# Kernel optimization log

Measured on AMD Instinct MI355X. Metric: run time of the kernel, lower is better.

## Reference

```python
import jax, jax.numpy as jnp
import numpy as np

B, S, D, H = 2, 2048, 1024, 16
HD = D // H
SCALE = HD ** -0.5

def setup_inputs() -> dict:
    key = jax.random.key(0)
    ks = jax.random.split(key, 3)
    x = jax.random.normal(ks[0], (B, S, D), dtype=jnp.float32)
    Wqkv = jax.random.normal(ks[1], (D, 3 * D), dtype=jnp.float32) * (D ** -0.5)
    bqkv = jnp.zeros((3 * D,), dtype=jnp.float32)
    Wproj = jax.random.normal(ks[2], (D, D), dtype=jnp.float32) * (D ** -0.5)
    bproj = jnp.zeros((D,), dtype=jnp.float32)
    return {"x": x, "Wqkv": Wqkv, "bqkv": bqkv, "Wproj": Wproj, "bproj": bproj}

def reference(x, Wqkv, bqkv, Wproj, bproj):
    b, s, d = x.shape
    qkv = x @ Wqkv + bqkv                       # (b, s, 3d)
    qkv = qkv.reshape(b, s, 3, H, HD)
    q, k, v = (qkv[:, :, 0], qkv[:, :, 1], qkv[:, :, 2])  # (b, s, h, hd)
    # scores: (b, h, s, s)
    attn = jnp.einsum('bqhd,bkhd->bhqk', q, k) * SCALE
    attn = jax.nn.softmax(attn, axis=-1)
    out = jnp.einsum('bhqk,bkhd->bqhd', attn, v).reshape(b, s, d)
    out = out @ Wproj + bproj
    return out
```

## Files before the change

### kernel.cpp

```cpp
#include <hip/hip_runtime.h>

typedef __attribute__((ext_vector_type(8))) short bf16x8;
typedef __attribute__((ext_vector_type(4))) float f32x4;
typedef __attribute__((ext_vector_type(16))) float f32x16;
typedef unsigned short u16;
typedef unsigned int u32;

#define MFMA16(a,b,c) __builtin_amdgcn_mfma_f32_16x16x32_bf16((a),(b),(c),0,0,0)
#define MFMA32(a,b,c) __builtin_amdgcn_mfma_f32_32x32x16_bf16((a),(b),(c),0,0,0)

#if __has_builtin(__builtin_amdgcn_exp2f)
#define EXP2(x) __builtin_amdgcn_exp2f(x)
#else
#define EXP2(x) __expf((x) * 0.6931471805599453f)
#endif

__device__ __forceinline__ u16 f2bf(float f) {
  u32 u = __builtin_bit_cast(u32, f);
  u += 0x7FFFu + ((u >> 16) & 1u);
  return (u16)(u >> 16);
}

__device__ __forceinline__ u32 cvtpk(float lo, float hi) {
  u32 r;
  asm("v_cvt_pk_bf16_f32 %0, %1, %2" : "=v"(r) : "v"(lo), "v"(hi));
  return r;
}

__device__ __forceinline__ void swap32(u32& a, u32& b) {
#if __has_builtin(__builtin_amdgcn_permlane32_swap)
  auto r = __builtin_amdgcn_permlane32_swap((int)a, (int)b, false, false);
  a = (u32)r[0];
  b = (u32)r[1];
#else
  u32 pa = __shfl_xor(a, 32), pb = __shfl_xor(b, 32);
  bool lo = ((threadIdx.x & 32) == 0);
  u32 na = lo ? a : pb;
  u32 nb = lo ? pa : b;
  a = na; b = nb;
#endif
}

__device__ __forceinline__ void gload16(const u16* g, u16* l) {
  __builtin_amdgcn_global_load_lds(
      (const __attribute__((address_space(1))) u32*)(const void*)g,
      (__attribute__((address_space(3))) u32*)(void*)l, 16, 0, 0);
}

__device__ __forceinline__ bf16x8 ldsfrag(const u16* lds, int row, int chunk) {
  return *(const bf16x8*)(lds + row * 64 + ((chunk ^ (row & 7)) << 3));
}

__global__ __launch_bounds__(256) void convert_x(const float* __restrict__ in,
                                                 u16* __restrict__ out, int n4) {
  int i = blockIdx.x * blockDim.x + threadIdx.x;
  int stride = gridDim.x * blockDim.x;
  for (; i < n4; i += stride) {
    float4 v = ((const float4*)in)[i];
    u32 lo = (u32)f2bf(v.x) | ((u32)f2bf(v.y) << 16);
    u32 hi = (u32)f2bf(v.z) | ((u32)f2bf(v.w) << 16);
    uint2 pv; pv.x = lo; pv.y = hi;
    ((uint2*)out)[i] = pv;
  }
}

__global__ __launch_bounds__(256) void transpose_w(const float* __restrict__ in,
                                                   u16* __restrict__ out,
                                                   int R, int C) {
  __shared__ float t[32][33];
  int c0 = blockIdx.x * 32, r0 = blockIdx.y * 32;
  int tc = threadIdx.x & 31, tr = threadIdx.x >> 5;
#pragma unroll
  for (int j = 0; j < 4; ++j) {
    int r = tr + j * 8;
    t[r][tc] = in[(size_t)(r0 + r) * C + c0 + tc];
  }
  __syncthreads();
#pragma unroll
  for (int j = 0; j < 4; ++j) {
    int cc = tr + j * 8;
    out[(size_t)(c0 + cc) * R + r0 + tc] = f2bf(t[tc][cc]);
  }
}

template <int MODE>
__global__ __launch_bounds__(256, 3) void gemm_k(
    const u16* __restrict__ A, const u16* __restrict__ Bt,
    const float* __restrict__ bias,
    u16* __restrict__ Qo, u16* __restrict__ Ko, u16* __restrict__ Vt,
    float* __restrict__ Of) {
  __shared__ alignas(16) u16 As[3][4096];
  __shared__ alignas(16) u16 Bs[3][4096];
  const int tid = threadIdx.x;
  const int wid = tid >> 6, lane = tid & 63;
  const int g = lane >> 4, lr = lane & 15;
  const int m0 = blockIdx.y * 128, n0 = blockIdx.x * 128;
  const int wr = (wid >> 1) * 64, wc = (wid & 1) * 64;

  f32x4 acc[4][4];
#pragma unroll
  for (int i = 0; i < 4; ++i)
#pragma unroll
    for (int j = 0; j < 4; ++j) acc[i][j] = (f32x4){0.f, 0.f, 0.f, 0.f};

  const u16* Ab = A + (size_t)m0 * 1024;
  const u16* Bb = Bt + (size_t)n0 * 1024;

  const int srow = tid >> 2, sc = tid & 3;
  auto stage = [&](int buf, int kt) {
#pragma unroll
    for (int i = 0; i < 2; ++i) {
      int s = tid + i * 256;
      int row = srow + i * 64;
      int csrc = sc ^ ((row >> 1) & 3);
      gload16(Ab + (size_t)row * 1024 + kt + csrc * 8, As[buf] + s * 8);
      gload16(Bb + (size_t)row * 1024 + kt + csrc * 8, Bs[buf] + s * 8);
    }
  };

  stage(0, 0);
  stage(1, 32);
  int cur = 0;
  for (int ki = 0; ki < 32; ++ki) {
    if (ki + 2 < 32) {
      int nxt = cur + 2; if (nxt >= 3) nxt -= 3;
      stage(nxt, (ki + 2) * 32);
    }
    if (ki < 30)       asm volatile("s_waitcnt vmcnt(8)" ::: "memory");
    else if (ki == 30) asm volatile("s_waitcnt vmcnt(4)" ::: "memory");
    else               asm volatile("s_waitcnt vmcnt(0)" ::: "memory");
    __builtin_amdgcn_sched_barrier(0);
    __builtin_amdgcn_s_barrier();
    __builtin_amdgcn_sched_barrier(0);

    bf16x8 af[4], bfr[4];
#pragma unroll
    for (int i = 0; i < 4; ++i) {
      int row = wr + i * 16 + lr;
      int slot = g ^ ((row >> 1) & 3);
      af[i] = *(const bf16x8*)(As[cur] + row * 32 + slot * 8);
    }
#pragma unroll
    for (int j = 0; j < 4; ++j) {
      int row = wc + j * 16 + lr;
      int slot = g ^ ((row >> 1) & 3);
      bfr[j] = *(const bf16x8*)(Bs[cur] + row * 32 + slot * 8);
    }
    __builtin_amdgcn_s_setprio(1);
#pragma unroll
    for (int i = 0; i < 4; ++i)
#pragma unroll
      for (int j = 0; j < 4; ++j)
        acc[i][j] = MFMA16(af[i], bfr[j], acc[i][j]);
    __builtin_amdgcn_s_setprio(0);

    __builtin_amdgcn_s_barrier();
    __builtin_amdgcn_sched_barrier(0);
    cur += 1; if (cur >= 3) cur -= 3;
  }

  if constexpr (MODE == 1) {
#pragma unroll
    for (int i = 0; i < 4; ++i) {
      int row = m0 + wr + i * 16 + g * 4;
#pragma unroll
      for (int j = 0; j < 4; ++j) {
        int col = n0 + wc + j * 16 + lr;
        float bv = bias[col];
#pragma unroll
        for (int r = 0; r < 4; ++r)
          Of[(size_t)(row + r) * 1024 + col] = acc[i][j][r] + bv;
      }
    }
  } else {
    const int sel = n0 >> 10;
#pragma unroll
    for (int i = 0; i < 4; ++i) {
      int row = m0 + wr + i * 16 + g * 4;
      int b = row >> 11, s = row & 2047;
#pragma unroll
      for (int j = 0; j < 4; ++j) {
        int col = n0 + wc + j * 16 + lr;
        float bv = bias[col];
        int nn = col & 1023;
        int h = nn >> 6, hd = nn & 63;
        if (sel == 2) {
          u16 pk[4];
#pragma unroll
          for (int r = 0; r < 4; ++r) pk[r] = f2bf(acc[i][j][r] + bv);
          uint2 pv;
          pv.x = (u32)pk[0] | ((u32)pk[1] << 16);
          pv.y = (u32)pk[2] | ((u32)pk[3] << 16);
          *(uint2*)(Vt + (size_t)((b * 16 + h) * 64 + hd) * 2048 + s) = pv;
        } else {
          u16* dst = (sel == 0) ? Qo : Ko;
#pragma unroll
          for (int r = 0; r < 4; ++r)
            dst[(size_t)((b * 16 + h) * 2048 + s + r) * 64 + hd] =
                f2bf(acc[i][j][r] + bv);
        }
      }
    }
  }
}

__global__ __launch_bounds__(256, 2) void attn_k(const u16* __restrict__ Q,
                                                 const u16* __restrict__ K,
                                                 const u16* __restrict__ Vt,
                                                 u16* __restrict__ O) {
  __shared__ alignas(16) u16 Ks[3][4096];
  __shared__ alignas(16) u16 Vs[3][4096];
  const int tid = threadIdx.x;
  const int wid = tid >> 6, lane = tid & 63;
  const int l31 = lane & 31, b5 = lane >> 5;
  const int p = blockIdx.x;
  const int l = (p & 7) * 64 + (p >> 3);
  const int qt = l & 15, bh = l >> 4;
  const u16* Qh = Q + (size_t)bh * 2048 * 64;
  const u16* Kh = K + (size_t)bh * 2048 * 64;
  const u16* Vh = Vt + (size_t)bh * 64 * 2048;

  const int qbase = qt * 128 + wid * 32;
  const u16* qp = Qh + (size_t)(qbase + l31) * 64 + b5 * 8;
  bf16x8 qf[4];
#pragma unroll
  for (int c = 0; c < 4; ++c) qf[c] = *(const bf16x8*)(qp + 16 * c);
  __builtin_amdgcn_sched_barrier(0);

  auto stage = [&](int buf, int t) {
#pragma unroll
    for (int i = 0; i < 2; ++i) {
      int s = tid + i * 256;
      int row = s >> 3, c = (s & 7) ^ (row & 7);
      gload16(Kh + (t * 64 + row) * 64 + c * 8, Ks[buf] + s * 8);
      gload16(Vh + row * 2048 + t * 64 + c * 8, Vs[buf] + s * 8);
    }
  };
  stage(0, 0);
  stage(1, 1);

  f32x16 accO0, accO1;
#pragma unroll
  for (int r = 0; r < 16; ++r) { accO0[r] = 0.f; accO1[r] = 0.f; }
  float mraw = -1e30f;
  float mC = 0.f;
  float lsum = 0.f;

  const float C2 = 0.125f * 1.44269504088896f;

  int cur = 0;
  for (int t = 0; t < 32; ++t) {
    if (t + 2 < 32) {
      int nxt = cur + 2; if (nxt >= 3) nxt -= 3;
      stage(nxt, t + 2);
    }
    if (t < 30)       asm volatile("s_waitcnt vmcnt(8)" ::: "memory");
    else if (t == 30) asm volatile("s_waitcnt vmcnt(4)" ::: "memory");
    else              asm volatile("s_waitcnt vmcnt(0)" ::: "memory");
    __builtin_amdgcn_sched_barrier(0);
    __builtin_amdgcn_s_barrier();
    __builtin_amdgcn_sched_barrier(0);

    const u16* Kc = Ks[cur];
    const u16* Vc = Vs[cur];

    f32x16 s0, s1;
#pragma unroll
    for (int r = 0; r < 16; ++r) { s0[r] = 0.f; s1[r] = 0.f; }
    __builtin_amdgcn_s_setprio(1);
#pragma unroll
    for (int c = 0; c < 4; ++c) {
      bf16x8 k0 = ldsfrag(Kc, l31, 2 * c + b5);
      bf16x8 k1 = ldsfrag(Kc, 32 + l31, 2 * c + b5);
      s0 = MFMA32(k0, qf[c], s0);
      s1 = MFMA32(k1, qf[c], s1);
    }
    __builtin_amdgcn_s_setprio(0);

    float rmax;
    {
      float a0 = fmaxf(fmaxf(s0[0], s0[1]), fmaxf(s0[2], s0[3]));
      float a1 = fmaxf(fmaxf(s0[4], s0[5]), fmaxf(s0[6], s0[7]));
      float a2 = fmaxf(fmaxf(s0[8], s0[9]), fmaxf(s0[10], s0[11]));
      float a3 = fmaxf(fmaxf(s0[12], s0[13]), fmaxf(s0[14], s0[15]));
      float b0 = fmaxf(fmaxf(s1[0], s1[1]), fmaxf(s1[2], s1[3]));
      float b1 = fmaxf(fmaxf(s1[4], s1[5]), fmaxf(s1[6], s1[7]));
      float b2 = fmaxf(fmaxf(s1[8], s1[9]), fmaxf(s1[10], s1[11]));
      float b3 = fmaxf(fmaxf(s1[12], s1[13]), fmaxf(s1[14], s1[15]));
      rmax = fmaxf(fmaxf(fmaxf(a0, a1), fmaxf(a2, a3)),
                   fmaxf(fmaxf(b0, b1), fmaxf(b2, b3)));
    }
    rmax = fmaxf(rmax, __shfl_xor(rmax, 32));

    if (__any(rmax > mraw + 64.f)) {
      float mn = fmaxf(mraw, rmax);
      float al = EXP2((mraw - mn) * C2);
      mraw = mn;
      mC = mn * C2;
      lsum *= al;
#pragma unroll
      for (int r = 0; r < 16; ++r) {
        accO0[r] *= al;
        accO1[r] *= al;
      }
    }

    u32 w0[8], w1[8];
#pragma unroll
    for (int i = 0; i < 8; ++i) {
      float p0 = EXP2(__builtin_fmaf(s0[2 * i], C2, -mC));
      float p1 = EXP2(__builtin_fmaf(s0[2 * i + 1], C2, -mC));
      float p2 = EXP2(__builtin_fmaf(s1[2 * i], C2, -mC));
      float p3 = EXP2(__builtin_fmaf(s1[2 * i + 1], C2, -mC));
      lsum += (p0 + p1) + (p2 + p3);
      w0[i] = cvtpk(p0, p1);
      w1[i] = cvtpk(p2, p3);
    }

    __builtin_amdgcn_s_setprio(1);
#pragma unroll
    for (int c = 0; c < 4; ++c) {
      u32 a0, a1, b0, b1;
      if (c == 0)      { a0 = w0[0]; b0 = w0[2]; a1 = w0[1]; b1 = w0[3]; }
      else if (c == 1) { a0 = w0[4]; b0 = w0[6]; a1 = w0[5]; b1 = w0[7]; }
      else if (c == 2) { a0 = w1[0]; b0 = w1[2]; a1 = w1[1]; b1 = w1[3]; }
      else             { a0 = w1[4]; b0 = w1[6]; a1 = w1[5]; b1 = w1[7]; }
      swap32(a0, b0);
      swap32(a1, b1);
      uint4 u; u.x = a0; u.y = a1; u.z = b0; u.w = b1;
      bf16x8 pf = __builtin_bit_cast(bf16x8, u);
      bf16x8 v0 = ldsfrag(Vc, l31, 2 * c + b5);
      bf16x8 v1 = ldsfrag(Vc, 32 + l31, 2 * c + b5);
      accO0 = MFMA32(v0, pf, accO0);
      accO1 = MFMA32(v1, pf, accO1);
    }
    __builtin_amdgcn_s_setprio(0);

    __builtin_amdgcn_s_barrier();
    __builtin_amdgcn_sched_barrier(0);
    cur += 1; if (cur >= 3) cur -= 3;
  }

  float ls = lsum + __shfl_xor(lsum, 32);
  float inv = 1.f / ls;
  const int b = bh >> 4, h = bh & 15;
  u16* orow = O + (size_t)(b * 2048 + qbase + l31) * 1024 + h * 64;
#pragma unroll
  for (int rg = 0; rg < 4; ++rg) {
    int hd0 = 8 * rg + 4 * b5;
    uint2 o0, o1;
    o0.x = cvtpk(accO0[4 * rg + 0] * inv, accO0[4 * rg + 1] * inv);
    o0.y = cvtpk(accO0[4 * rg + 2] * inv, accO0[4 * rg + 3] * inv);
    o1.x = cvtpk(accO1[4 * rg + 0] * inv, accO1[4 * rg + 1] * inv);
    o1.y = cvtpk(accO1[4 * rg + 2] * inv, accO1[4 * rg + 3] * inv);
    *(uint2*)(orow + hd0) = o0;
    *(uint2*)(orow + 32 + hd0) = o1;
  }
}

extern "C" void kernel_launch(void* const* d_in, const int* in_sizes, int n_in,
                              void* d_out, int out_size, void* d_ws, size_t ws_size,
                              hipStream_t stream) {
  (void)in_sizes; (void)n_in; (void)out_size; (void)ws_size;
  const float* x = (const float*)d_in[0];
  const float* Wqkv = (const float*)d_in[1];
  const float* bqkv = (const float*)d_in[2];
  const float* Wproj = (const float*)d_in[3];
  const float* bproj = (const float*)d_in[4];
  float* out = (float*)d_out;

  char* ws = (char*)d_ws;
  size_t off = 0;
  auto alloc = [&](size_t bytes) {
    void* p = ws + off;
    off += (bytes + 255) & ~(size_t)255;
    return p;
  };
  u16* xb     = (u16*)alloc((size_t)4096 * 1024 * 2);
  u16* Wqkvt  = (u16*)alloc((size_t)3072 * 1024 * 2);
  u16* Wprojt = (u16*)alloc((size_t)1024 * 1024 * 2);
  u16* Qb     = (u16*)alloc((size_t)32 * 2048 * 64 * 2);
  u16* Kb     = (u16*)alloc((size_t)32 * 2048 * 64 * 2);
  u16* Vtb    = (u16*)alloc((size_t)32 * 64 * 2048 * 2);
  u16* AOb    = (u16*)alloc((size_t)4096 * 1024 * 2);

  convert_x<<<2048, 256, 0, stream>>>(x, xb, 4096 * 1024 / 4);
  transpose_w<<<dim3(96, 32), 256, 0, stream>>>(Wqkv, Wqkvt, 1024, 3072);
  transpose_w<<<dim3(32, 32), 256, 0, stream>>>(Wproj, Wprojt, 1024, 1024);
  gemm_k<0><<<dim3(24, 32), 256, 0, stream>>>(xb, Wqkvt, bqkv, Qb, Kb, Vtb, nullptr);
  attn_k<<<512, 256, 0, stream>>>(Qb, Kb, Vtb, AOb);
  gemm_k<1><<<dim3(8, 32), 256, 0, stream>>>(AOb, Wprojt, bproj, nullptr, nullptr, nullptr, out);
}
```

Measured before the change: 128.1 us.

## Split attention KV range across waves with per-wave buffers and LDS combine

```diff
diff --git a/kernel.cpp b/kernel.cpp
--- a/kernel.cpp
+++ b/kernel.cpp
@@ -49,6 +49,9 @@
 
 __device__ __forceinline__ bf16x8 ldsfrag(const u16* lds, int row, int chunk) {
   return *(const bf16x8*)(lds + row * 64 + ((chunk ^ (row & 7)) << 3));
+}
+__device__ __forceinline__ bf16x8 ldsfragV(const u16* lds, int row, int chunk) {
+  return *(const bf16x8*)(lds + row * 32 + ((chunk ^ (row & 3)) << 3));
 }
 
 __global__ __launch_bounds__(256) void convert_x(const float* __restrict__ in,
@@ -208,32 +211,42 @@
                                                  const u16* __restrict__ K,
                                                  const u16* __restrict__ Vt,
                                                  u16* __restrict__ O) {
-  __shared__ alignas(16) u16 Ks[3][4096];
-  __shared__ alignas(16) u16 Vs[3][4096];
+  __shared__ alignas(16) u16 SM[32768];
   const int tid = threadIdx.x;
   const int wid = tid >> 6, lane = tid & 63;
   const int l31 = lane & 31, b5 = lane >> 5;
   const int p = blockIdx.x;
-  const int l = (p & 7) * 64 + (p >> 3);
-  const int qt = l & 15, bh = l >> 4;
+  const int l = (p & 7) * 256 + (p >> 3);
+  const int qt = l & 63, bh = l >> 6;
   const u16* Qh = Q + (size_t)bh * 2048 * 64;
   const u16* Kh = K + (size_t)bh * 2048 * 64;
   const u16* Vh = Vt + (size_t)bh * 64 * 2048;
 
-  const int qbase = qt * 128 + wid * 32;
+  const int qbase = qt * 32;
   const u16* qp = Qh + (size_t)(qbase + l31) * 64 + b5 * 8;
   bf16x8 qf[4];
 #pragma unroll
   for (int c = 0; c < 4; ++c) qf[c] = *(const bf16x8*)(qp + 16 * c);
   __builtin_amdgcn_sched_barrier(0);
 
-  auto stage = [&](int buf, int t) {
-#pragma unroll
-    for (int i = 0; i < 2; ++i) {
-      int s = tid + i * 256;
+  u16* mybuf = SM + wid * 8192;
+  const int kvw = wid * 512;
+
+  auto stage = [&](int b, int t) {
+    int kv0 = kvw + t * 32;
+    u16* Kb = mybuf + b * 4096;
+    u16* Vb = Kb + 2048;
+#pragma unroll
+    for (int i = 0; i < 4; ++i) {
+      int s = lane + i * 64;
       int row = s >> 3, c = (s & 7) ^ (row & 7);
-      gload16(Kh + (t * 64 + row) * 64 + c * 8, Ks[buf] + s * 8);
-      gload16(Vh + row * 2048 + t * 64 + c * 8, Vs[buf] + s * 8);
+      gload16(Kh + (size_t)(kv0 + row) * 64 + c * 8, Kb + s * 8);
+    }
+#pragma unroll
+    for (int i = 0; i < 4; ++i) {
+      int s = lane + i * 64;
+      int row = s >> 2, c = (s & 3) ^ (row & 3);
+      gload16(Vh + (size_t)row * 2048 + kv0 + c * 8, Vb + s * 8);
     }
   };
   stage(0, 0);
@@ -248,32 +261,22 @@
 
   const float C2 = 0.125f * 1.44269504088896f;
 
-  int cur = 0;
-  for (int t = 0; t < 32; ++t) {
-    if (t + 2 < 32) {
-      int nxt = cur + 2; if (nxt >= 3) nxt -= 3;
-      stage(nxt, t + 2);
-    }
-    if (t < 30)       asm volatile("s_waitcnt vmcnt(8)" ::: "memory");
-    else if (t == 30) asm volatile("s_waitcnt vmcnt(4)" ::: "memory");
-    else              asm volatile("s_waitcnt vmcnt(0)" ::: "memory");
+  for (int t = 0; t < 16; ++t) {
+    if (t < 15) asm volatile("s_waitcnt vmcnt(8)" ::: "memory");
+    else        asm volatile("s_waitcnt vmcnt(0)" ::: "memory");
     __builtin_amdgcn_sched_barrier(0);
-    __builtin_amdgcn_s_barrier();
-    __builtin_amdgcn_sched_barrier(0);
-
-    const u16* Kc = Ks[cur];
-    const u16* Vc = Vs[cur];
-
-    f32x16 s0, s1;
-#pragma unroll
-    for (int r = 0; r < 16; ++r) { s0[r] = 0.f; s1[r] = 0.f; }
+
+    const u16* Kc = mybuf + (t & 1) * 4096;
+    const u16* Vc = Kc + 2048;
+
+    f32x16 s0;
+#pragma unroll
+    for (int r = 0; r < 16; ++r) s0[r] = 0.f;
     __builtin_amdgcn_s_setprio(1);
 #pragma unroll
     for (int c = 0; c < 4; ++c) {
       bf16x8 k0 = ldsfrag(Kc, l31, 2 * c + b5);
-      bf16x8 k1 = ldsfrag(Kc, 32 + l31, 2 * c + b5);
       s0 = MFMA32(k0, qf[c], s0);
-      s1 = MFMA32(k1, qf[c], s1);
     }
     __builtin_amdgcn_s_setprio(0);
 
@@ -283,12 +286,7 @@
       float a1 = fmaxf(fmaxf(s0[4], s0[5]), fmaxf(s0[6], s0[7]));
       float a2 = fmaxf(fmaxf(s0[8], s0[9]), fmaxf(s0[10], s0[11]));
       float a3 = fmaxf(fmaxf(s0[12], s0[13]), fmaxf(s0[14], s0[15]));
-      float b0 = fmaxf(fmaxf(s1[0], s1[1]), fmaxf(s1[2], s1[3]));
-      float b1 = fmaxf(fmaxf(s1[4], s1[5]), fmaxf(s1[6], s1[7]));
-      float b2 = fmaxf(fmaxf(s1[8], s1[9]), fmaxf(s1[10], s1[11]));
-      float b3 = fmaxf(fmaxf(s1[12], s1[13]), fmaxf(s1[14], s1[15]));
-      rmax = fmaxf(fmaxf(fmaxf(a0, a1), fmaxf(a2, a3)),
-                   fmaxf(fmaxf(b0, b1), fmaxf(b2, b3)));
+      rmax = fmaxf(fmaxf(a0, a1), fmaxf(a2, a3));
     }
     rmax = fmaxf(rmax, __shfl_xor(rmax, 32));
 
@@ -305,56 +303,65 @@
       }
     }
 
-    u32 w0[8], w1[8];
+    u32 w0[8];
 #pragma unroll
     for (int i = 0; i < 8; ++i) {
       float p0 = EXP2(__builtin_fmaf(s0[2 * i], C2, -mC));
       float p1 = EXP2(__builtin_fmaf(s0[2 * i + 1], C2, -mC));
-      float p2 = EXP2(__builtin_fmaf(s1[2 * i], C2, -mC));
-      float p3 = EXP2(__builtin_fmaf(s1[2 * i + 1], C2, -mC));
-      lsum += (p0 + p1) + (p2 + p3);
+      lsum += p0 + p1;
       w0[i] = cvtpk(p0, p1);
-      w1[i] = cvtpk(p2, p3);
     }
 
     __builtin_amdgcn_s_setprio(1);
 #pragma unroll
-    for (int c = 0; c < 4; ++c) {
+    for (int c = 0; c < 2; ++c) {
       u32 a0, a1, b0, b1;
-      if (c == 0)      { a0 = w0[0]; b0 = w0[2]; a1 = w0[1]; b1 = w0[3]; }
-      else if (c == 1) { a0 = w0[4]; b0 = w0[6]; a1 = w0[5]; b1 = w0[7]; }
-      else if (c == 2) { a0 = w1[0]; b0 = w1[2]; a1 = w1[1]; b1 = w1[3]; }
-      else             { a0 = w1[4]; b0 = w1[6]; a1 = w1[5]; b1 = w1[7]; }
+      if (c == 0) { a0 = w0[0]; b0 = w0[2]; a1 = w0[1]; b1 = w0[3]; }
+      else        { a0 = w0[4]; b0 = w0[6]; a1 = w0[5]; b1 = w0[7]; }
       swap32(a0, b0);
       swap32(a1, b1);
       uint4 u; u.x = a0; u.y = a1; u.z = b0; u.w = b1;
       bf16x8 pf = __builtin_bit_cast(bf16x8, u);
-      bf16x8 v0 = ldsfrag(Vc, l31, 2 * c + b5);
-      bf16x8 v1 = ldsfrag(Vc, 32 + l31, 2 * c + b5);
+      bf16x8 v0 = ldsfragV(Vc, l31, 2 * c + b5);
+      bf16x8 v1 = ldsfragV(Vc, 32 + l31, 2 * c + b5);
       accO0 = MFMA32(v0, pf, accO0);
       accO1 = MFMA32(v1, pf, accO1);
     }
     __builtin_amdgcn_s_setprio(0);
 
-    __builtin_amdgcn_s_barrier();
-    __builtin_amdgcn_sched_barrier(0);
-    cur += 1; if (cur >= 3) cur -= 3;
+    if (t + 2 < 16) stage(t & 1, t + 2);
   }
 
   float ls = lsum + __shfl_xor(lsum, 32);
-  float inv = 1.f / ls;
+  __syncthreads();
+
+  float* Om = (float*)SM;
+  float2* mlp = (float2*)(SM + 17408);
+  if (b5 == 0) mlp[wid * 32 + l31] = make_float2(mraw, ls);
+  float* myOm = Om + wid * 2176;
+#pragma unroll
+  for (int r = 0; r < 16; ++r) {
+    int hd = (r & 3) + 8 * (r >> 2) + 4 * b5;
+    myOm[hd * 34 + l31] = accO0[r];
+    myOm[(32 + hd) * 34 + l31] = accO1[r];
+  }
+  __syncthreads();
+
   const int b = bh >> 4, h = bh & 15;
-  u16* orow = O + (size_t)(b * 2048 + qbase + l31) * 1024 + h * 64;
-#pragma unroll
-  for (int rg = 0; rg < 4; ++rg) {
-    int hd0 = 8 * rg + 4 * b5;
-    uint2 o0, o1;
-    o0.x = cvtpk(accO0[4 * rg + 0] * inv, accO0[4 * rg + 1] * inv);
-    o0.y = cvtpk(accO0[4 * rg + 2] * inv, accO0[4 * rg + 3] * inv);
-    o1.x = cvtpk(accO1[4 * rg + 0] * inv, accO1[4 * rg + 1] * inv);
-    o1.y = cvtpk(accO1[4 * rg + 2] * inv, accO1[4 * rg + 3] * inv);
-    *(uint2*)(orow + hd0) = o0;
-    *(uint2*)(orow + 32 + hd0) = o1;
+  const int hd = tid & 63;
+#pragma unroll
+  for (int k = 0; k < 8; ++k) {
+    int q = (tid >> 6) + 4 * k;
+    float2 ml0 = mlp[q], ml1 = mlp[32 + q], ml2 = mlp[64 + q], ml3 = mlp[96 + q];
+    float M = fmaxf(fmaxf(ml0.x, ml1.x), fmaxf(ml2.x, ml3.x));
+    float u0 = EXP2((ml0.x - M) * C2);
+    float u1 = EXP2((ml1.x - M) * C2);
+    float u2 = EXP2((ml2.x - M) * C2);
+    float u3 = EXP2((ml3.x - M) * C2);
+    float inv = 1.f / (u0 * ml0.y + u1 * ml1.y + u2 * ml2.y + u3 * ml3.y);
+    float o = u0 * Om[hd * 34 + q] + u1 * Om[2176 + hd * 34 + q] +
+              u2 * Om[4352 + hd * 34 + q] + u3 * Om[6528 + hd * 34 + q];
+    O[(size_t)(b * 2048 + qbase + q) * 1024 + h * 64 + hd] = f2bf(o * inv);
   }
 }
 
@@ -388,6 +395,6 @@
   transpose_w<<<dim3(96, 32), 256, 0, stream>>>(Wqkv, Wqkvt, 1024, 3072);
   transpose_w<<<dim3(32, 32), 256, 0, stream>>>(Wproj, Wprojt, 1024, 1024);
   gemm_k<0><<<dim3(24, 32), 256, 0, stream>>>(xb, Wqkvt, bqkv, Qb, Kb, Vtb, nullptr);
-  attn_k<<<512, 256, 0, stream>>>(Qb, Kb, Vtb, AOb);
+  attn_k<<<2048, 256, 0, stream>>>(Qb, Kb, Vtb, AOb);
   gemm_k<1><<<dim3(8, 32), 256, 0, stream>>>(AOb, Wprojt, bproj, nullptr, nullptr, nullptr, out);
 }
```

Result: slower. 149.1 us (+16.4%).
